# Optimization experiments

Measured on AMD Instinct MI355X. Metric: run time of the kernel, lower is better.

Reference implementation:

```python
import jax, jax.numpy as jnp
import numpy as np

B, L, E, S, V = 256, 64, 128, 16, 50000
H0, H1 = 16 * E, 4 * E  # dense hidden sizes from dense_sequence_lengths [64,16,4]
PAD_IDX, UNK_IDX = 1, 0


def setup_inputs() -> dict:
    key = jax.random.key(0)
    ks = jax.random.split(key, 12)
    text_lengths = jax.random.randint(ks[0], (B,), 1, L + 1)
    text_lengths = text_lengths.at[0].set(L)  # ensure max(lengths) == L
    raw_tokens = jax.random.randint(ks[1], (B, L), 2, V)
    pos = jnp.arange(L)
    text_batch = jnp.where(pos[None, :] < text_lengths[:, None], raw_tokens, PAD_IDX)
    sentiment_ids = jax.random.randint(ks[2], (B,), 0, 2)

    emb_table = jax.random.normal(ks[3], (V, E), dtype=jnp.float32) * 0.1
    emb_table = emb_table.at[UNK_IDX].set(0.0).at[PAD_IDX].set(0.0)
    sentiment_table = jax.random.normal(ks[4], (2, S), dtype=jnp.float32)
    sentiment_table = sentiment_table / jnp.linalg.norm(sentiment_table, axis=1, keepdims=True)

    D_in = L * E + S + E  # 8336
    W0 = jax.random.normal(ks[5], (D_in, H0), dtype=jnp.float32) * 0.02
    b0 = jax.random.normal(ks[6], (H0,), dtype=jnp.float32) * 0.02
    W1 = jax.random.normal(ks[7], (H0, H1), dtype=jnp.float32) * 0.02
    b1 = jax.random.normal(ks[8], (H1,), dtype=jnp.float32) * 0.02
    Wp = jax.random.normal(ks[9], (H1, 1), dtype=jnp.float32) * 0.02
    bp = jax.random.normal(ks[10], (1,), dtype=jnp.float32) * 0.02
    return {"text_batch": text_batch, "text_lengths": text_lengths,
            "sentiment_ids": sentiment_ids, "emb_table": emb_table,
            "sentiment_table": sentiment_table, "W0": W0, "b0": b0,
            "W1": W1, "b1": b1, "Wp": Wp, "bp": bp}


def reference(text_batch, text_lengths, sentiment_ids, emb_table, sentiment_table,
              W0, b0, W1, b1, Wp, bp):
    # nn.Embedding(max_norm=1.0): renorm rows with norm > 1 (torch uses eps 1e-7)
    norms = jnp.linalg.norm(emb_table, axis=1, keepdims=True)
    w = emb_table * jnp.where(norms > 1.0, 1.0 / (norms + 1e-7), 1.0)
    emb = w[text_batch]                       # (B, L, E)  (dropout is identity in eval)
    sent_flat = emb.reshape(B, L * E)         # flattened sentence embedding
    sv = sentiment_table[sentiment_ids]       # (B, S)

    # First dense layer on concat([sent_flat, sv, word_emb]) factored so the
    # shared sentence/sentiment part is computed once per sentence.
    W_sent, W_snt, W_word = W0[:L * E], W0[L * E:L * E + S], W0[L * E + S:]
    base = sent_flat @ W_sent + sv @ W_snt + b0            # (B, H0)
    h0 = jax.nn.relu(base[:, None, :] + jnp.einsum('ble,eh->blh', emb, W_word))  # (B, L, H0)
    h1 = jax.nn.relu(jnp.einsum('blh,hk->blk', h0, W1) + b1)                      # (B, L, H1)

    # Positions >= text_length keep their zero initialization in encoded_batch
    mask = jnp.arange(L)[None, :] < text_lengths[:, None]  # (B, L)
    enc = jnp.where(mask[:, :, None], h1, 0.0)

    pred = jax.nn.sigmoid(enc @ Wp + bp)[..., 0]           # (B, L)
    return pred
```

## Files before the change

### kernel.cpp

```cpp
#include <hip/hip_runtime.h>
#include <hip/hip_bf16.h>

#define B_   256
#define L_   64
#define E_   128
#define S_   16
#define H0_  2048
#define H1_  512
#define LE_  8192
#define DIN_ 8336
#define NROW 16384

typedef __attribute__((ext_vector_type(8))) short short8_t;
typedef __attribute__((ext_vector_type(4))) float f32x4;

static __device__ __forceinline__ f32x4 mfma16(short8_t a, short8_t b, f32x4 c){
  return __builtin_amdgcn_mfma_f32_16x16x32_bf16(a, b, c, 0, 0, 0);
}

static __device__ __forceinline__ unsigned short f2bf(float x){
  unsigned u = __builtin_bit_cast(unsigned, x);
  unsigned r = u + 0x7FFFu + ((u >> 16) & 1u);
  return (unsigned short)(r >> 16);
}

static __device__ __forceinline__ void gl_lds16(const void* g, void* l){
  __builtin_amdgcn_global_load_lds((const __attribute__((address_space(1))) unsigned*)g,
                                   (__attribute__((address_space(3))) unsigned*)l, 16, 0, 0);
}

__global__ __launch_bounds__(256) void k_scan(const int* __restrict__ lens,
    int* __restrict__ rowmap, int* __restrict__ offs, int* __restrict__ meta){
  __shared__ int sh[256];
  int t = threadIdx.x;
  int v = lens[t];
  sh[t] = v;
  __syncthreads();
  for (int d = 1; d < 256; d <<= 1){
    int y = (t >= d) ? sh[t - d] : 0;
    __syncthreads();
    sh[t] += y;
    __syncthreads();
  }
  int off = sh[t] - v;
  int nv = sh[255];
  offs[t] = off;
  if (t == 0){ meta[0] = nv; meta[1] = (nv + 127) & ~127; }
  for (int l = 0; l < v; ++l) rowmap[off + l] = t * 64 + l;
  for (int i = nv + t; i < NROW; i += 256) rowmap[i] = 0;
}

__global__ __launch_bounds__(256) void k_transpose_cvt(const float* __restrict__ src,
    unsigned short* __restrict__ dst, int R, int C){
  __shared__ unsigned short tile[64][65];
  int R0 = blockIdx.x * 64, C0 = blockIdx.y * 64;
  int t = threadIdx.x;
  int row = t >> 2, c16 = (t & 3) * 16;
  int gr = R0 + row;
  if (gr < R){
    const float* p = src + (size_t)gr * C + C0 + c16;
    #pragma unroll
    for (int j = 0; j < 16; j += 4){
      float4 v = *reinterpret_cast<const float4*>(p + j);
      tile[row][c16+j+0] = f2bf(v.x);
      tile[row][c16+j+1] = f2bf(v.y);
      tile[row][c16+j+2] = f2bf(v.z);
      tile[row][c16+j+3] = f2bf(v.w);
    }
  }
  __syncthreads();
  int orow = t >> 2, r16 = (t & 3) * 16;
  unsigned short buf[16];
  #pragma unroll
  for (int j = 0; j < 16; ++j) buf[j] = tile[r16 + j][orow];
  unsigned short* q = dst + (size_t)(C0 + orow) * R + R0 + r16;
  if (R0 + r16 + 15 < R){
    *reinterpret_cast<short8_t*>(q)     = *reinterpret_cast<short8_t*>(&buf[0]);
    *reinterpret_cast<short8_t*>(q + 8) = *reinterpret_cast<short8_t*>(&buf[8]);
  } else {
    for (int j = 0; j < 16; ++j) if (R0 + r16 + j < R) q[j] = buf[j];
  }
}

__global__ __launch_bounds__(256) void k_gather(const int* __restrict__ tokens,
    const float* __restrict__ emb, unsigned short* __restrict__ ebf){
  int wid  = blockIdx.x * 4 + (threadIdx.x >> 6);
  int lane = threadIdx.x & 63;
  int tok  = tokens[wid];
  const float* row = emb + (size_t)tok * E_;
  float2 v = *reinterpret_cast<const float2*>(row + lane * 2);
  float ss = v.x * v.x + v.y * v.y;
  #pragma unroll
  for (int m = 1; m < 64; m <<= 1) ss += __shfl_xor(ss, m, 64);
  float nrm = sqrtf(ss);
  float scale = (nrm > 1.0f) ? 1.0f / (nrm + 1e-7f) : 1.0f;
  unsigned a = f2bf(v.x * scale), b = f2bf(v.y * scale);
  *reinterpret_cast<unsigned*>(ebf + (size_t)wid * E_ + lane * 2) = a | (b << 16);
}

__global__ __launch_bounds__(256) void k_gemmA(const unsigned short* __restrict__ ebf,
    const unsigned short* __restrict__ W0T, float* __restrict__ part){
  __shared__ unsigned short Al[64*64];
  __shared__ unsigned short Bl[128*64];
  int bid = blockIdx.x;
  int mt = bid & 3, nt = (bid >> 2) & 15, kw = bid >> 6;
  int m0 = mt * 64, n0 = nt * 128, k0 = kw * 2048;
  int t = threadIdx.x, lane = t & 63, w = t >> 6;
  int wm = w >> 1, wn = w & 1;
  f32x4 acc[2][4];
  #pragma unroll
  for (int m = 0; m < 2; ++m)
    #pragma unroll
    for (int n = 0; n < 4; ++n) acc[m][n] = (f32x4){0.f,0.f,0.f,0.f};

  for (int it = 0; it < 32; ++it){
    int kb = k0 + it * 64;
    __syncthreads();
    #pragma unroll
    for (int c = 0; c < 2; ++c){
      int q = w * 2 + c;
      int row = q * 8 + (lane >> 3);
      gl_lds16(ebf + (size_t)(m0 + row) * LE_ + kb + (lane & 7) * 8, &Al[q * 512]);
    }
    #pragma unroll
    for (int c = 0; c < 4; ++c){
      int q = w * 4 + c;
      int row = q * 8 + (lane >> 3);
      gl_lds16(W0T + (size_t)(n0 + row) * DIN_ + kb + (lane & 7) * 8, &Bl[q * 512]);
    }
    __syncthreads();
    #pragma unroll
    for (int ks = 0; ks < 2; ++ks){
      short8_t af[2], bfr[4];
      #pragma unroll
      for (int m = 0; m < 2; ++m)
        af[m] = *reinterpret_cast<const short8_t*>(&Al[(wm*32 + m*16 + (lane & 15))*64 + ks*32 + (lane >> 4)*8]);
      #pragma unroll
      for (int n = 0; n < 4; ++n)
        bfr[n] = *reinterpret_cast<const short8_t*>(&Bl[(wn*64 + n*16 + (lane & 15))*64 + ks*32 + (lane >> 4)*8]);
      #pragma unroll
      for (int m = 0; m < 2; ++m)
        #pragma unroll
        for (int n = 0; n < 4; ++n) acc[m][n] = mfma16(af[m], bfr[n], acc[m][n]);
    }
  }
  float* P = part + (size_t)kw * B_ * H0_;
  #pragma unroll
  for (int m = 0; m < 2; ++m)
    #pragma unroll
    for (int n = 0; n < 4; ++n)
      #pragma unroll
      for (int i = 0; i < 4; ++i){
        int r = m0 + wm*32 + m*16 + (lane >> 4)*4 + i;
        int c = n0 + wn*64 + n*16 + (lane & 15);
        P[(size_t)r * H0_ + c] = acc[m][n][i];
      }
}

__global__ __launch_bounds__(256) void k_base(const int* __restrict__ sid,
    const float* __restrict__ stab, const float* __restrict__ W0,
    const float* __restrict__ b0, const float* __restrict__ part,
    float* __restrict__ base){
  int idx = blockIdx.x * 256 + threadIdx.x;
  int b = idx >> 11, h = idx & 2047;
  const float* sv = stab + sid[b] * S_;
  float acc = b0[h];
  #pragma unroll
  for (int s = 0; s < S_; ++s) acc += sv[s] * W0[(size_t)(LE_ + s) * H0_ + h];
  #pragma unroll
  for (int kw = 0; kw < 4; ++kw) acc += part[(size_t)kw * B_ * H0_ + idx];
  base[idx] = acc;
}

__global__ __launch_bounds__(256) void k_h0(const unsigned short* __restrict__ ebf,
    const unsigned short* __restrict__ W0T, const float* __restrict__ base,
    const int* __restrict__ rowmap, const int* __restrict__ meta,
    unsigned short* __restrict__ h0c){
  int m0 = blockIdx.x * 128;
  if (m0 >= meta[1]) return;
  int n0 = blockIdx.y * 128;
  __shared__ char smem[65536];
  unsigned short* Alds = (unsigned short*)smem;
  unsigned short* Blds = (unsigned short*)(smem + 32768);
  int t = threadIdx.x, lane = t & 63, w = t >> 6;
  int wm = w >> 1, wn = w & 1;

  #pragma unroll
  for (int c = 0; c < 8; ++c){
    int q = w * 8 + c;
    int row = q * 4 + (lane >> 4);
    int rm = rowmap[m0 + row];
    gl_lds16(ebf + (size_t)rm * E_ + (lane & 15) * 8, &Alds[q * 512]);
  }
  #pragma unroll
  for (int c = 0; c < 8; ++c){
    int q = w * 8 + c;
    int row = q * 4 + (lane >> 4);
    gl_lds16(W0T + (size_t)(n0 + row) * DIN_ + (LE_ + S_) + (lane & 15) * 8, &Blds[q * 512]);
  }
  __syncthreads();

  f32x4 acc[4][4];
  #pragma unroll
  for (int m = 0; m < 4; ++m)
    #pragma unroll
    for (int n = 0; n < 4; ++n) acc[m][n] = (f32x4){0.f,0.f,0.f,0.f};
  #pragma unroll
  for (int ks = 0; ks < 4; ++ks){
    short8_t af[4], bfr[4];
    #pragma unroll
    for (int m = 0; m < 4; ++m)
      af[m] = *reinterpret_cast<const short8_t*>(&Alds[(wm*64 + m*16 + (lane & 15))*128 + ks*32 + (lane >> 4)*8]);
    #pragma unroll
    for (int n = 0; n < 4; ++n)
      bfr[n] = *reinterpret_cast<const short8_t*>(&Blds[(wn*64 + n*16 + (lane & 15))*128 + ks*32 + (lane >> 4)*8]);
    #pragma unroll
    for (int m = 0; m < 4; ++m)
      #pragma unroll
      for (int n = 0; n < 4; ++n) acc[m][n] = mfma16(af[m], bfr[n], acc[m][n]);
  }
  __syncthreads();
  unsigned short* Hs = (unsigned short*)smem;
  #pragma unroll
  for (int m = 0; m < 4; ++m)
    #pragma unroll
    for (int i = 0; i < 4; ++i){
      int row_l = wm*64 + m*16 + (lane >> 4)*4 + i;
      int rm = rowmap[m0 + row_l];
      const float* bb = base + (size_t)(rm >> 6) * H0_ + n0;
      #pragma unroll
      for (int n = 0; n < 4; ++n){
        int col_l = wn*64 + n*16 + (lane & 15);
        float vv = acc[m][n][i] + bb[col_l];
        Hs[row_l * 136 + col_l] = f2bf(vv > 0.f ? vv : 0.f);
      }
    }
  __syncthreads();
  int row = t >> 1, half = t & 1;
  const unsigned short* hp = Hs + row * 136 + half * 64;
  unsigned short* gp = h0c + (size_t)(m0 + row) * H0_ + n0 + half * 64;
  #pragma unroll
  for (int j = 0; j < 8; ++j)
    *reinterpret_cast<short8_t*>(gp + j * 8) = *reinterpret_cast<const short8_t*>(hp + j * 8);
}

__global__ __launch_bounds__(256) void k_h1(const unsigned short* __restrict__ h0c,
    const unsigned short* __restrict__ W1T, const float* __restrict__ b1,
    const float* __restrict__ Wp, const int* __restrict__ meta,
    float* __restrict__ logitc){
  int m0 = blockIdx.x * 128;
  if (m0 >= meta[1]) return;
  int n0 = blockIdx.y * 128;
  __shared__ unsigned short Al[128*64];
  __shared__ unsigned short Bl[128*64];
  int t = threadIdx.x, lane = t & 63, w = t >> 6;
  int wm = w >> 1, wn = w & 1;
  f32x4 acc[4][4];
  #pragma unroll
  for (int m = 0; m < 4; ++m)
    #pragma unroll
    for (int n = 0; n < 4; ++n) acc[m][n] = (f32x4){0.f,0.f,0.f,0.f};

  for (int it = 0; it < 32; ++it){
    int kb = it * 64;
    __syncthreads();
    #pragma unroll
    for (int c = 0; c < 4; ++c){
      int q = w * 4 + c;
      int row = q * 8 + (lane >> 3);
      gl_lds16(h0c + (size_t)(m0 + row) * H0_ + kb + (lane & 7) * 8, &Al[q * 512]);
    }
    #pragma unroll
    for (int c = 0; c < 4; ++c){
      int q = w * 4 + c;
      int row = q * 8 + (lane >> 3);
      gl_lds16(W1T + (size_t)(n0 + row) * H0_ + kb + (lane & 7) * 8, &Bl[q * 512]);
    }
    __syncthreads();
    #pragma unroll
    for (int ks = 0; ks < 2; ++ks){
      short8_t af[4], bfr[4];
      #pragma unroll
      for (int m = 0; m < 4; ++m)
        af[m] = *reinterpret_cast<const short8_t*>(&Al[(wm*64 + m*16 + (lane & 15))*64 + ks*32 + (lane >> 4)*8]);
      #pragma unroll
      for (int n = 0; n < 4; ++n)
        bfr[n] = *reinterpret_cast<const short8_t*>(&Bl[(wn*64 + n*16 + (lane & 15))*64 + ks*32 + (lane >> 4)*8]);
      #pragma unroll
      for (int m = 0; m < 4; ++m)
        #pragma unroll
        for (int n = 0; n < 4; ++n) acc[m][n] = mfma16(af[m], bfr[n], acc[m][n]);
    }
  }
  float b1v[4], wpv[4];
  #pragma unroll
  for (int n = 0; n < 4; ++n){
    int col = n0 + wn*64 + n*16 + (lane & 15);
    b1v[n] = b1[col]; wpv[n] = Wp[col];
  }
  #pragma unroll
  for (int m = 0; m < 4; ++m)
    #pragma unroll
    for (int i = 0; i < 4; ++i){
      float p = 0.f;
      #pragma unroll
      for (int n = 0; n < 4; ++n){
        float h = acc[m][n][i] + b1v[n];
        h = h > 0.f ? h : 0.f;
        p += h * wpv[n];
      }
      p += __shfl_xor(p, 1); p += __shfl_xor(p, 2);
      p += __shfl_xor(p, 4); p += __shfl_xor(p, 8);
      if ((lane & 15) == 0)
        atomicAdd(&logitc[m0 + wm*64 + m*16 + (lane >> 4)*4 + i], p);
    }
}

__global__ __launch_bounds__(256) void k_finish(const int* __restrict__ lens,
    const int* __restrict__ offs, const float* __restrict__ logitc,
    const float* __restrict__ bp, float* __restrict__ out){
  int idx = blockIdx.x * 256 + threadIdx.x;
  int b = idx >> 6, l = idx & 63;
  float x = bp[0];
  if (l < lens[b]) x += logitc[offs[b] + l];
  out[idx] = 1.f / (1.f + expf(-x));
}

extern "C" void kernel_launch(void* const* d_in, const int* in_sizes, int n_in,
                              void* d_out, int out_size, void* d_ws, size_t ws_size,
                              hipStream_t stream){
  const int*   text = (const int*)d_in[0];
  const int*   lens = (const int*)d_in[1];
  const int*   sid  = (const int*)d_in[2];
  const float* emb  = (const float*)d_in[3];
  const float* stab = (const float*)d_in[4];
  const float* W0   = (const float*)d_in[5];
  const float* b0   = (const float*)d_in[6];
  const float* W1   = (const float*)d_in[7];
  const float* b1   = (const float*)d_in[8];
  const float* Wp   = (const float*)d_in[9];
  const float* bp   = (const float*)d_in[10];
  float* out = (float*)d_out;

  char* ws = (char*)d_ws;
  unsigned short* ebf    = (unsigned short*)(ws);
  unsigned short* W0T    = (unsigned short*)(ws + 4194304);
  unsigned short* W1T    = (unsigned short*)(ws + 38338560);
  float*          base   = (float*)(ws + 40435712);
  float*          part   = (float*)(ws + 42532864);
  float*          logitc = (float*)(ws + 50921472);
  int*            rowmap = (int*)(ws + 50987008);
  int*            offs   = (int*)(ws + 51052544);
  int*            meta   = (int*)(ws + 51053568);
  unsigned short* h0c    = (unsigned short*)(ws + 51054592);

  hipMemsetAsync(logitc, 0, NROW * 4, stream);
  hipLaunchKernelGGL(k_scan,      dim3(1),        dim3(256), 0, stream, lens, rowmap, offs, meta);
  hipLaunchKernelGGL(k_gather,    dim3(4096),     dim3(256), 0, stream, text, emb, ebf);
  hipLaunchKernelGGL(k_transpose_cvt, dim3(131, 32), dim3(256), 0, stream, W0, W0T, DIN_, H0_);
  hipLaunchKernelGGL(k_transpose_cvt, dim3(32, 8),   dim3(256), 0, stream, W1, W1T, H0_, H1_);
  hipLaunchKernelGGL(k_gemmA,     dim3(256),      dim3(256), 0, stream, ebf, W0T, part);
  hipLaunchKernelGGL(k_base,      dim3(2048),     dim3(256), 0, stream, sid, stab, W0, b0, part, base);
  hipLaunchKernelGGL(k_h0,        dim3(128, 16),  dim3(256), 0, stream, ebf, W0T, base, rowmap, meta, h0c);
  hipLaunchKernelGGL(k_h1,        dim3(128, 4),   dim3(256), 0, stream, h0c, W1T, b1, Wp, meta, logitc);
  hipLaunchKernelGGL(k_finish,    dim3(64),       dim3(256), 0, stream, lens, offs, logitc, bp, out);
}
```

Measured before the change: 285.1 us.

## Double-buffer LDS in GEMM kernels, add XOR swizzle, shrink h1 M-tile

The k_gemmA and k_h1 main loops now use double-buffered LDS, so the next K-slice is prefetched while MFMAs run on the current one. The global-to-LDS copies and the fragment reads use an XOR column swizzle, also applied in k_h0, to cut LDS bank conflicts. k_h1 moves from 128-row to 64-row M tiles on a doubled grid, with a separate 64-aligned row count in meta, to raise parallelism and occupancy. The cost is more LDS per block, and the halved tile lowers data reuse per block in k_h1.

```diff
diff --git a/kernel.cpp b/kernel.cpp
--- a/kernel.cpp
+++ b/kernel.cpp
@@ -45,7 +45,11 @@
   int off = sh[t] - v;
   int nv = sh[255];
   offs[t] = off;
-  if (t == 0){ meta[0] = nv; meta[1] = (nv + 127) & ~127; }
+  if (t == 0){
+    meta[0] = nv;
+    meta[1] = (nv + 63) & ~63;
+    meta[2] = (nv + 127) & ~127;
+  }
   for (int l = 0; l < v; ++l) rowmap[off + l] = t * 64 + l;
   for (int i = nv + t; i < NROW; i += 256) rowmap[i] = 0;
 }
@@ -98,51 +102,64 @@
   *reinterpret_cast<unsigned*>(ebf + (size_t)wid * E_ + lane * 2) = a | (b << 16);
 }
 
-__global__ __launch_bounds__(256) void k_gemmA(const unsigned short* __restrict__ ebf,
+static __device__ __forceinline__ void stage64(
+    const unsigned short* __restrict__ Asrc, size_t strideA, int m0,
+    const unsigned short* __restrict__ Bsrc, size_t strideB, int n0,
+    int kbA, int kbB, int w, int lane,
+    unsigned short* Al, unsigned short* Bl){
+  int rsub = lane >> 3;
+  int csw  = 8 * ((lane & 7) ^ rsub);
+  #pragma unroll
+  for (int c = 0; c < 2; ++c){
+    int q = w * 2 + c;
+    gl_lds16(Asrc + (size_t)(m0 + q*8 + rsub) * strideA + kbA + csw, Al + q * 512);
+  }
+  #pragma unroll
+  for (int c = 0; c < 4; ++c){
+    int q = w * 4 + c;
+    gl_lds16(Bsrc + (size_t)(n0 + q*8 + rsub) * strideB + kbB + csw, Bl + q * 512);
+  }
+}
+
+__global__ __launch_bounds__(256, 2) void k_gemmA(const unsigned short* __restrict__ ebf,
     const unsigned short* __restrict__ W0T, float* __restrict__ part){
-  __shared__ unsigned short Al[64*64];
-  __shared__ unsigned short Bl[128*64];
+  __shared__ unsigned short Al[2][64*64];
+  __shared__ unsigned short Bl[2][128*64];
   int bid = blockIdx.x;
   int mt = bid & 3, nt = (bid >> 2) & 15, kw = bid >> 6;
   int m0 = mt * 64, n0 = nt * 128, k0 = kw * 2048;
   int t = threadIdx.x, lane = t & 63, w = t >> 6;
   int wm = w >> 1, wn = w & 1;
+  int sw = (lane & 7) * 8, hi = (lane >> 4) * 8, fr = lane & 15;
   f32x4 acc[2][4];
   #pragma unroll
   for (int m = 0; m < 2; ++m)
     #pragma unroll
     for (int n = 0; n < 4; ++n) acc[m][n] = (f32x4){0.f,0.f,0.f,0.f};
 
+  stage64(ebf, LE_, m0, W0T, DIN_, n0, k0, k0, w, lane, Al[0], Bl[0]);
+  __syncthreads();
   for (int it = 0; it < 32; ++it){
-    int kb = k0 + it * 64;
-    __syncthreads();
-    #pragma unroll
-    for (int c = 0; c < 2; ++c){
-      int q = w * 2 + c;
-      int row = q * 8 + (lane >> 3);
-      gl_lds16(ebf + (size_t)(m0 + row) * LE_ + kb + (lane & 7) * 8, &Al[q * 512]);
-    }
-    #pragma unroll
-    for (int c = 0; c < 4; ++c){
-      int q = w * 4 + c;
-      int row = q * 8 + (lane >> 3);
-      gl_lds16(W0T + (size_t)(n0 + row) * DIN_ + kb + (lane & 7) * 8, &Bl[q * 512]);
-    }
-    __syncthreads();
+    int cur = it & 1;
+    if (it + 1 < 32)
+      stage64(ebf, LE_, m0, W0T, DIN_, n0, k0 + (it+1)*64, k0 + (it+1)*64,
+              w, lane, Al[cur^1], Bl[cur^1]);
     #pragma unroll
     for (int ks = 0; ks < 2; ++ks){
+      int col = (ks*32 + hi) ^ sw;
       short8_t af[2], bfr[4];
       #pragma unroll
       for (int m = 0; m < 2; ++m)
-        af[m] = *reinterpret_cast<const short8_t*>(&Al[(wm*32 + m*16 + (lane & 15))*64 + ks*32 + (lane >> 4)*8]);
+        af[m] = *reinterpret_cast<const short8_t*>(&Al[cur][(wm*32 + m*16 + fr)*64 + col]);
       #pragma unroll
       for (int n = 0; n < 4; ++n)
-        bfr[n] = *reinterpret_cast<const short8_t*>(&Bl[(wn*64 + n*16 + (lane & 15))*64 + ks*32 + (lane >> 4)*8]);
+        bfr[n] = *reinterpret_cast<const short8_t*>(&Bl[cur][(wn*64 + n*16 + fr)*64 + col]);
       #pragma unroll
       for (int m = 0; m < 2; ++m)
         #pragma unroll
         for (int n = 0; n < 4; ++n) acc[m][n] = mfma16(af[m], bfr[n], acc[m][n]);
     }
+    __syncthreads();
   }
   float* P = part + (size_t)kw * B_ * H0_;
   #pragma unroll
@@ -152,7 +169,7 @@
       #pragma unroll
       for (int i = 0; i < 4; ++i){
         int r = m0 + wm*32 + m*16 + (lane >> 4)*4 + i;
-        int c = n0 + wn*64 + n*16 + (lane & 15);
+        int c = n0 + wn*64 + n*16 + fr;
         P[(size_t)r * H0_ + c] = acc[m][n][i];
       }
 }
@@ -172,31 +189,38 @@
   base[idx] = acc;
 }
 
-__global__ __launch_bounds__(256) void k_h0(const unsigned short* __restrict__ ebf,
+__global__ __launch_bounds__(256, 2) void k_h0(const unsigned short* __restrict__ ebf,
     const unsigned short* __restrict__ W0T, const float* __restrict__ base,
     const int* __restrict__ rowmap, const int* __restrict__ meta,
     unsigned short* __restrict__ h0c){
   int m0 = blockIdx.x * 128;
-  if (m0 >= meta[1]) return;
+  if (m0 >= meta[2]) return;
   int n0 = blockIdx.y * 128;
   __shared__ char smem[65536];
   unsigned short* Alds = (unsigned short*)smem;
   unsigned short* Blds = (unsigned short*)(smem + 32768);
   int t = threadIdx.x, lane = t & 63, w = t >> 6;
   int wm = w >> 1, wn = w & 1;
-
-  #pragma unroll
-  for (int c = 0; c < 8; ++c){
-    int q = w * 8 + c;
-    int row = q * 4 + (lane >> 4);
-    int rm = rowmap[m0 + row];
-    gl_lds16(ebf + (size_t)rm * E_ + (lane & 15) * 8, &Alds[q * 512]);
-  }
-  #pragma unroll
-  for (int c = 0; c < 8; ++c){
-    int q = w * 8 + c;
-    int row = q * 4 + (lane >> 4);
-    gl_lds16(W0T + (size_t)(n0 + row) * DIN_ + (LE_ + S_) + (lane & 15) * 8, &Blds[q * 512]);
+  int sw = (lane & 7) * 8, hi = (lane >> 4) * 8, fr = lane & 15;
+
+  {
+    int rsub = lane >> 4;
+    int bc = lane & 15;
+    #pragma unroll
+    for (int c = 0; c < 8; ++c){
+      int q = w * 8 + c;
+      int row7 = (q & 1) * 4 + rsub;
+      int csw = 8 * (bc ^ row7);
+      int rm = rowmap[m0 + q*4 + rsub];
+      gl_lds16(ebf + (size_t)rm * E_ + csw, Alds + q * 512);
+    }
+    #pragma unroll
+    for (int c = 0; c < 8; ++c){
+      int q = w * 8 + c;
+      int row7 = (q & 1) * 4 + rsub;
+      int csw = 8 * (bc ^ row7);
+      gl_lds16(W0T + (size_t)(n0 + q*4 + rsub) * DIN_ + (LE_ + S_) + csw, Blds + q * 512);
+    }
   }
   __syncthreads();
 
@@ -207,13 +231,14 @@
     for (int n = 0; n < 4; ++n) acc[m][n] = (f32x4){0.f,0.f,0.f,0.f};
   #pragma unroll
   for (int ks = 0; ks < 4; ++ks){
+    int col = (ks*32 + hi) ^ sw;
     short8_t af[4], bfr[4];
     #pragma unroll
     for (int m = 0; m < 4; ++m)
-      af[m] = *reinterpret_cast<const short8_t*>(&Alds[(wm*64 + m*16 + (lane & 15))*128 + ks*32 + (lane >> 4)*8]);
+      af[m] = *reinterpret_cast<const short8_t*>(&Alds[(wm*64 + m*16 + fr)*128 + col]);
     #pragma unroll
     for (int n = 0; n < 4; ++n)
-      bfr[n] = *reinterpret_cast<const short8_t*>(&Blds[(wn*64 + n*16 + (lane & 15))*128 + ks*32 + (lane >> 4)*8]);
+      bfr[n] = *reinterpret_cast<const short8_t*>(&Blds[(wn*64 + n*16 + fr)*128 + col]);
     #pragma unroll
     for (int m = 0; m < 4; ++m)
       #pragma unroll
@@ -230,7 +255,7 @@
       const float* bb = base + (size_t)(rm >> 6) * H0_ + n0;
       #pragma unroll
       for (int n = 0; n < 4; ++n){
-        int col_l = wn*64 + n*16 + (lane & 15);
+        int col_l = wn*64 + n*16 + fr;
         float vv = acc[m][n][i] + bb[col_l];
         Hs[row_l * 136 + col_l] = f2bf(vv > 0.f ? vv : 0.f);
       }
@@ -244,62 +269,55 @@
     *reinterpret_cast<short8_t*>(gp + j * 8) = *reinterpret_cast<const short8_t*>(hp + j * 8);
 }
 
-__global__ __launch_bounds__(256) void k_h1(const unsigned short* __restrict__ h0c,
+__global__ __launch_bounds__(256, 2) void k_h1(const unsigned short* __restrict__ h0c,
     const unsigned short* __restrict__ W1T, const float* __restrict__ b1,
     const float* __restrict__ Wp, const int* __restrict__ meta,
     float* __restrict__ logitc){
-  int m0 = blockIdx.x * 128;
+  int m0 = blockIdx.x * 64;
   if (m0 >= meta[1]) return;
   int n0 = blockIdx.y * 128;
-  __shared__ unsigned short Al[128*64];
-  __shared__ unsigned short Bl[128*64];
+  __shared__ unsigned short Al[2][64*64];
+  __shared__ unsigned short Bl[2][128*64];
   int t = threadIdx.x, lane = t & 63, w = t >> 6;
   int wm = w >> 1, wn = w & 1;
-  f32x4 acc[4][4];
-  #pragma unroll
-  for (int m = 0; m < 4; ++m)
+  int sw = (lane & 7) * 8, hi = (lane >> 4) * 8, fr = lane & 15;
+  f32x4 acc[2][4];
+  #pragma unroll
+  for (int m = 0; m < 2; ++m)
     #pragma unroll
     for (int n = 0; n < 4; ++n) acc[m][n] = (f32x4){0.f,0.f,0.f,0.f};
 
+  stage64(h0c, H0_, m0, W1T, H0_, n0, 0, 0, w, lane, Al[0], Bl[0]);
+  __syncthreads();
   for (int it = 0; it < 32; ++it){
-    int kb = it * 64;
-    __syncthreads();
-    #pragma unroll
-    for (int c = 0; c < 4; ++c){
-      int q = w * 4 + c;
-      int row = q * 8 + (lane >> 3);
-      gl_lds16(h0c + (size_t)(m0 + row) * H0_ + kb + (lane & 7) * 8, &Al[q * 512]);
-    }
-    #pragma unroll
-    for (int c = 0; c < 4; ++c){
-      int q = w * 4 + c;
-      int row = q * 8 + (lane >> 3);
-      gl_lds16(W1T + (size_t)(n0 + row) * H0_ + kb + (lane & 7) * 8, &Bl[q * 512]);
-    }
-    __syncthreads();
+    int cur = it & 1;
+    if (it + 1 < 32)
+      stage64(h0c, H0_, m0, W1T, H0_, n0, (it+1)*64, (it+1)*64, w, lane, Al[cur^1], Bl[cur^1]);
     #pragma unroll
     for (int ks = 0; ks < 2; ++ks){
-      short8_t af[4], bfr[4];
-      #pragma unroll
-      for (int m = 0; m < 4; ++m)
-        af[m] = *reinterpret_cast<const short8_t*>(&Al[(wm*64 + m*16 + (lane & 15))*64 + ks*32 + (lane >> 4)*8]);
+      int col = (ks*32 + hi) ^ sw;
+      short8_t af[2], bfr[4];
+      #pragma unroll
+      for (int m = 0; m < 2; ++m)
+        af[m] = *reinterpret_cast<const short8_t*>(&Al[cur][(wm*32 + m*16 + fr)*64 + col]);
       #pragma unroll
       for (int n = 0; n < 4; ++n)
-        bfr[n] = *reinterpret_cast<const short8_t*>(&Bl[(wn*64 + n*16 + (lane & 15))*64 + ks*32 + (lane >> 4)*8]);
-      #pragma unroll
-      for (int m = 0; m < 4; ++m)
+        bfr[n] = *reinterpret_cast<const short8_t*>(&Bl[cur][(wn*64 + n*16 + fr)*64 + col]);
+      #pragma unroll
+      for (int m = 0; m < 2; ++m)
         #pragma unroll
         for (int n = 0; n < 4; ++n) acc[m][n] = mfma16(af[m], bfr[n], acc[m][n]);
     }
+    __syncthreads();
   }
   float b1v[4], wpv[4];
   #pragma unroll
   for (int n = 0; n < 4; ++n){
-    int col = n0 + wn*64 + n*16 + (lane & 15);
+    int col = n0 + wn*64 + n*16 + fr;
     b1v[n] = b1[col]; wpv[n] = Wp[col];
   }
   #pragma unroll
-  for (int m = 0; m < 4; ++m)
+  for (int m = 0; m < 2; ++m)
     #pragma unroll
     for (int i = 0; i < 4; ++i){
       float p = 0.f;
@@ -312,7 +330,7 @@
       p += __shfl_xor(p, 1); p += __shfl_xor(p, 2);
       p += __shfl_xor(p, 4); p += __shfl_xor(p, 8);
       if ((lane & 15) == 0)
-        atomicAdd(&logitc[m0 + wm*64 + m*16 + (lane >> 4)*4 + i], p);
+        atomicAdd(&logitc[m0 + wm*32 + m*16 + (lane >> 4)*4 + i], p);
     }
 }
 
@@ -362,6 +380,6 @@
   hipLaunchKernelGGL(k_gemmA,     dim3(256),      dim3(256), 0, stream, ebf, W0T, part);
   hipLaunchKernelGGL(k_base,      dim3(2048),     dim3(256), 0, stream, sid, stab, W0, b0, part, base);
   hipLaunchKernelGGL(k_h0,        dim3(128, 16),  dim3(256), 0, stream, ebf, W0T, base, rowmap, meta, h0c);
-  hipLaunchKernelGGL(k_h1,        dim3(128, 4),   dim3(256), 0, stream, h0c, W1T, b1, Wp, meta, logitc);
+  hipLaunchKernelGGL(k_h1,        dim3(256, 4),   dim3(256), 0, stream, h0c, W1T, b1, Wp, meta, logitc);
   hipLaunchKernelGGL(k_finish,    dim3(64),       dim3(256), 0, stream, lens, offs, logitc, bp, out);
 }
```

Result: faster. 250.8 us (-12.0%).
